# Performance work log

Measured on AMD Instinct MI355X. Metric: run time of the kernel, lower is better.

The kernel has to match this reference:

```python
import jax, jax.numpy as jnp
import numpy as np
from jax import lax

IMG = 800.0
PRE_NMS = 2000
POST_NMS = 1000
IOU_T = 0.7
BBOX_XFORM_CLIP = float(np.log(1000.0 / 16.0))


def build_anchors():
    # torchvision FPN anchor generator: one size per level, 3 aspect ratios
    strides = [4, 8, 16, 32, 64]
    sizes = [32, 64, 128, 256, 512]
    ratios = [0.5, 1.0, 2.0]
    out = []
    for s, sz in zip(strides, sizes):
        f = int(np.ceil(800 / s))  # feature map side
        base = []
        for r in ratios:
            w = sz * np.sqrt(1.0 / r)
            h = sz * np.sqrt(r)
            base.append([-w / 2, -h / 2, w / 2, h / 2])
        base = np.asarray(base)  # [3,4]
        sx = (np.arange(f) + 0.5) * s
        sy = (np.arange(f) + 0.5) * s
        yy, xx = np.meshgrid(sy, sx, indexing='ij')
        shifts = np.stack([xx, yy, xx, yy], -1).reshape(-1, 1, 4)
        out.append((shifts + base).reshape(-1, 4))
    return np.concatenate(out, 0).astype(np.float32)  # [159882,4]


def setup_inputs() -> dict:
    key = jax.random.key(0)
    k1, k2 = jax.random.split(key)
    B = 16
    anchors = jnp.asarray(build_anchors())
    A = anchors.shape[0]
    scores = jax.random.normal(k1, (B, A), dtype=jnp.float32)
    deltas = jax.random.normal(k2, (B, A, 4), dtype=jnp.float32) * 0.1
    return {"scores": scores, "deltas": deltas, "anchors": anchors}


def decode_boxes(deltas, anchors):
    wa = anchors[:, 2] - anchors[:, 0]
    ha = anchors[:, 3] - anchors[:, 1]
    cxa = anchors[:, 0] + 0.5 * wa
    cya = anchors[:, 1] + 0.5 * ha
    dx, dy = deltas[:, 0], deltas[:, 1]
    dw = jnp.minimum(deltas[:, 2], BBOX_XFORM_CLIP)
    dh = jnp.minimum(deltas[:, 3], BBOX_XFORM_CLIP)
    cx = dx * wa + cxa
    cy = dy * ha + cya
    w = jnp.exp(dw) * wa
    h = jnp.exp(dh) * ha
    boxes = jnp.stack([cx - 0.5 * w, cy - 0.5 * h, cx + 0.5 * w, cy + 0.5 * h], -1)
    return jnp.clip(boxes, 0.0, IMG)


def box_iou(a, b):
    # a: [N,4], b: [M,4]
    area_a = (a[:, 2] - a[:, 0]) * (a[:, 3] - a[:, 1])
    area_b = (b[:, 2] - b[:, 0]) * (b[:, 3] - b[:, 1])
    lt = jnp.maximum(a[:, None, :2], b[None, :, :2])
    rb = jnp.minimum(a[:, None, 2:], b[None, :, 2:])
    wh = jnp.clip(rb - lt, 0.0)
    inter = wh[..., 0] * wh[..., 1]
    return inter / (area_a[:, None] + area_b[None, :] - inter + 1e-9)


def greedy_nms_keep(boxes, iou_t):
    # boxes are sorted by descending score
    K = boxes.shape[0]
    iou = box_iou(boxes, boxes)  # [K,K]
    idx = jnp.arange(K)

    def body(i, keep):
        sup = (iou[i] > iou_t) & keep[i] & (idx > i)
        return keep & ~sup

    return lax.fori_loop(0, K, body, jnp.ones((K,), bool))


def _process_image(scores_i, deltas_i, anchors):
    # top-k pre-NMS on objectness logits (torchvision RPN order)
    top_logits, idx = lax.top_k(scores_i, PRE_NMS)
    boxes = decode_boxes(deltas_i[idx], anchors[idx])  # [PRE,4]
    keep = greedy_nms_keep(boxes, IOU_T)
    masked = jnp.where(keep, top_logits, -jnp.inf)
    kept_logits, idx2 = lax.top_k(masked, POST_NMS)
    kept_boxes = boxes[idx2]
    valid = jnp.isfinite(kept_logits)
    probs = jax.nn.sigmoid(jnp.where(valid, kept_logits, 0.0))
    out_boxes = jnp.where(valid[:, None], kept_boxes, 0.0)
    out_scores = jnp.where(valid, probs, 0.0)
    return jnp.concatenate([out_boxes, out_scores[:, None]], -1)  # [POST,5]


def reference(scores, deltas, anchors):
    return jax.vmap(_process_image, in_axes=(0, 0, None))(scores, deltas, anchors)
```

## Files before the change

kernel.cpp:

```cpp
#include <hip/hip_runtime.h>
#include <math.h>

#define PRE_NMS 2000
#define POST_NMS 1000
#define IOU_T 0.7f
#define IMGSZ 800.0f
#define CAP 6144
#define SORTN 2048
#define NBINS 1024
#define NWORDS 32
#define NSLICE 16
#define MROWS 2048
#define NTILES 528

typedef unsigned long long u64;

__device__ __forceinline__ unsigned key_of(float f) {
    unsigned u = __float_as_uint(f);
    return (u & 0x80000000u) ? ~u : (u | 0x80000000u);
}
__device__ __forceinline__ float inv_key(unsigned k) {
    unsigned u = (k & 0x80000000u) ? (k ^ 0x80000000u) : ~k;
    return __uint_as_float(u);
}

__global__ __launch_bounds__(256) void hist_kernel(
    const float* __restrict__ scores, int A, unsigned* __restrict__ ghist) {
  int b = blockIdx.x, slice = blockIdx.y;
  __shared__ unsigned h[NBINS];
  int tid = threadIdx.x;
  for (int i = tid; i < NBINS; i += 256) h[i] = 0;
  __syncthreads();
  int per = (A + NSLICE - 1) / NSLICE;
  int lo = slice * per, hi = min(lo + per, A);
  const float* sc = scores + (size_t)b * A;
  for (int i = lo + tid; i < hi; i += 256)
    atomicAdd(&h[key_of(sc[i]) >> 22], 1u);
  __syncthreads();
  for (int i = tid; i < NBINS; i += 256)
    if (h[i]) atomicAdd(&ghist[b * NBINS + i], h[i]);
}

__global__ __launch_bounds__(256) void compact_kernel(
    const float* __restrict__ scores, int A, const unsigned* __restrict__ ghist,
    u64* __restrict__ cand, int* __restrict__ cand_cnt, int* __restrict__ T1) {
  int b = blockIdx.x, slice = blockIdx.y;
  int tid = threadIdx.x;
  int lane = tid & 63, wave = tid >> 6;
  __shared__ unsigned sa[2][NBINS];
  __shared__ int sT;
  for (int i = tid; i < NBINS; i += 256) sa[0][i] = ghist[b * NBINS + i];
  __syncthreads();
  int src = 0;
  for (int d = 1; d < NBINS; d <<= 1) {
    for (int i = tid; i < NBINS; i += 256)
      sa[src ^ 1][i] = sa[src][i] + ((i + d < NBINS) ? sa[src][i + d] : 0u);
    __syncthreads();
    src ^= 1;
  }
  for (int i = tid; i < NBINS; i += 256) {
    unsigned v = sa[src][i];
    unsigned nx = (i < NBINS - 1) ? sa[src][i + 1] : 0u;
    if (v >= PRE_NMS && nx < PRE_NMS) sT = i;
  }
  __syncthreads();
  int T = sT;
  if (slice == 0 && tid == 0) T1[b] = T;
  int per = (A + NSLICE - 1) / NSLICE;
  int lo = slice * per, hi = min(lo + per, A);
  const float* sc = scores + (size_t)b * A;
  int cnt = 0;
  for (int i = lo + tid; i < hi; i += 256)
    cnt += ((int)(key_of(sc[i]) >> 22) >= T);
  int pfx = cnt;
  #pragma unroll
  for (int d = 1; d < 64; d <<= 1) {
    int t2 = __shfl_up(pfx, d, 64);
    if (lane >= d) pfx += t2;
  }
  __shared__ int s_wt[4];
  __shared__ int s_base;
  if (lane == 63) s_wt[wave] = pfx;
  __syncthreads();
  if (tid == 0) {
    int tot = s_wt[0] + s_wt[1] + s_wt[2] + s_wt[3];
    int acc = 0;
    #pragma unroll
    for (int w2 = 0; w2 < 4; ++w2) { int t3 = s_wt[w2]; s_wt[w2] = acc; acc += t3; }
    s_base = atomicAdd(&cand_cnt[b], tot);
  }
  __syncthreads();
  int my_off = s_base + s_wt[wave] + (pfx - cnt);
  u64* cb = cand + (size_t)b * CAP;
  for (int i = lo + tid; i < hi; i += 256) {
    unsigned k = key_of(sc[i]);
    if ((int)(k >> 22) >= T) {
      if (my_off < CAP) cb[my_off] = ((u64)k << 32) | (unsigned)(~i);
      my_off++;
    }
  }
}

__global__ __launch_bounds__(1024) void refine_select_kernel(
    const u64* __restrict__ cand, const int* __restrict__ cand_cnt,
    const int* __restrict__ T1,
    u64* __restrict__ gsel, int* __restrict__ sel_cnt) {
  int b = blockIdx.x, tid = threadIdx.x;
  int lane = tid & 63;
  __shared__ unsigned h2[NBINS];
  __shared__ unsigned tmp[NBINS];
  __shared__ int s_above, s_sel, s_T2;
  int n = min(cand_cnt[b], CAP);
  const u64* cb = cand + (size_t)b * CAP;
  h2[tid] = 0;
  if (tid == 0) { s_above = 0; s_sel = 0; }
  __syncthreads();
  int T1v = T1[b];
  int loc = 0;
  for (int i = tid; i < n; i += 1024) {
    unsigned k = (unsigned)(cb[i] >> 32);
    if ((int)(k >> 22) > T1v) loc++;
    else atomicAdd(&h2[(k >> 12) & 1023], 1u);
  }
  for (int d = 32; d; d >>= 1) loc += __shfl_down(loc, d, 64);
  if (lane == 0 && loc) atomicAdd(&s_above, loc);
  __syncthreads();
  unsigned v = h2[tid];
  for (int d = 1; d < NBINS; d <<= 1) {
    tmp[tid] = v;
    __syncthreads();
    if (tid + d < NBINS) v += tmp[tid + d];
    __syncthreads();
  }
  tmp[tid] = v;
  __syncthreads();
  int above = s_above;
  unsigned nextv = (tid < NBINS - 1) ? tmp[tid + 1] : 0u;
  if (above + (int)v >= PRE_NMS && above + (int)nextv < PRE_NMS) s_T2 = tid;
  __syncthreads();
  unsigned thresh20 = ((unsigned)T1v << 10) | (unsigned)s_T2;
  u64* gs = gsel + (size_t)b * SORTN;
  for (int i = tid; i < n; i += 1024) {
    u64 cv = cb[i];
    if ((unsigned)(cv >> 44) >= thresh20) {
      int pos = atomicAdd(&s_sel, 1);
      if (pos < SORTN) gs[pos] = cv;
    }
  }
  __syncthreads();
  if (tid == 0) sel_cnt[b] = min(s_sel, SORTN);
}

__global__ __launch_bounds__(256) void rank_decode_kernel(
    const u64* __restrict__ gsel, const int* __restrict__ sel_cnt,
    const float* __restrict__ deltas, const float* __restrict__ anchors, int A,
    float* __restrict__ boxes, float* __restrict__ topk_logit) {
  int b = blockIdx.x, ci = blockIdx.y;
  int tid = threadIdx.x;
  __shared__ u64 keys[SORTN];
  __shared__ int s_part[256];
  const u64* gs = gsel + (size_t)b * SORTN;
  int n = sel_cnt[b];
  for (int i = tid; i < SORTN; i += 256)
    keys[i] = (i < n) ? gs[i] : 0ULL;
  __syncthreads();
  int half = tid >> 7;
  int li = tid & 127;
  int i = ci * 128 + li;
  u64 my = keys[i];
  int rank = 0;
  const ulonglong2* k2 = (const ulonglong2*)(keys + half * (SORTN / 2));
  #pragma unroll 4
  for (int j = 0; j < SORTN / 4; ++j) {
    ulonglong2 kk = k2[j];
    rank += (kk.x > my) + (kk.y > my);
  }
  s_part[tid] = rank;
  __syncthreads();
  if (half == 0) {
    rank = s_part[tid] + s_part[tid + 128];
    if (i < n && rank < PRE_NMS) {
      int a = (int)(~(unsigned)my);
      topk_logit[b * PRE_NMS + rank] = inv_key((unsigned)(my >> 32));
      const float CLIP = 4.135166556742356f;
      float4 dl = ((const float4*)deltas)[(size_t)b * A + a];
      float4 an = ((const float4*)anchors)[a];
      float wa = __fsub_rn(an.z, an.x);
      float ha = __fsub_rn(an.w, an.y);
      float cxa = __fadd_rn(an.x, __fmul_rn(0.5f, wa));
      float cya = __fadd_rn(an.y, __fmul_rn(0.5f, ha));
      float dw = fminf(dl.z, CLIP), dh = fminf(dl.w, CLIP);
      float cx = __fadd_rn(__fmul_rn(dl.x, wa), cxa);
      float cy = __fadd_rn(__fmul_rn(dl.y, ha), cya);
      float w2 = __fmul_rn((float)exp((double)dw), wa);
      float h2f = __fmul_rn((float)exp((double)dh), ha);
      float x1 = __fsub_rn(cx, __fmul_rn(0.5f, w2));
      float y1 = __fsub_rn(cy, __fmul_rn(0.5f, h2f));
      float x2 = __fadd_rn(cx, __fmul_rn(0.5f, w2));
      float y2 = __fadd_rn(cy, __fmul_rn(0.5f, h2f));
      x1 = fminf(fmaxf(x1, 0.f), IMGSZ);
      y1 = fminf(fmaxf(y1, 0.f), IMGSZ);
      x2 = fminf(fmaxf(x2, 0.f), IMGSZ);
      y2 = fminf(fmaxf(y2, 0.f), IMGSZ);
      ((float4*)boxes)[(size_t)b * PRE_NMS + rank] = make_float4(x1, y1, x2, y2);
    }
  }
}

__global__ __launch_bounds__(64) void iou_tile(
    const float* __restrict__ boxes, u64* __restrict__ maskT,
    unsigned* __restrict__ tflag) {
  int k = blockIdx.x;
  int b = blockIdx.y;
  int wj = (int)((sqrtf(8.0f * k + 1.0f) - 1.0f) * 0.5f);
  while ((wj + 1) * (wj + 2) / 2 <= k) ++wj;
  while (wj * (wj + 1) / 2 > k) --wj;
  int ti = k - wj * (wj + 1) / 2;
  int lane = threadIdx.x;
  int i = ti * 64 + lane;
  const float4* bb = (const float4*)boxes + (size_t)b * PRE_NMS;
  __shared__ float4 sbox[64];
  int jg = wj * 64 + lane;
  sbox[lane] = bb[min(jg, PRE_NMS - 1)];
  float4 A4 = bb[min(i, PRE_NMS - 1)];
  __syncthreads();
  float area_a = __fmul_rn(__fsub_rn(A4.z, A4.x), __fsub_rn(A4.w, A4.y));
  u64 m = 0;
  #pragma unroll 8
  for (int jj = 0; jj < 64; ++jj) {
    float4 Bb = sbox[jj];
    float area_b = __fmul_rn(__fsub_rn(Bb.z, Bb.x), __fsub_rn(Bb.w, Bb.y));
    float ltx = fmaxf(A4.x, Bb.x), lty = fmaxf(A4.y, Bb.y);
    float rbx = fminf(A4.z, Bb.z), rby = fminf(A4.w, Bb.w);
    float iw = fmaxf(__fsub_rn(rbx, ltx), 0.f);
    float ih = fmaxf(__fsub_rn(rby, lty), 0.f);
    float inter = __fmul_rn(iw, ih);
    float denom = __fadd_rn(__fsub_rn(__fadd_rn(area_a, area_b), inter), 1e-9f);
    float iou = inter / denom;
    int j = wj * 64 + jj;
    if (j > i && iou > IOU_T) m |= 1ULL << jj;
  }
  maskT[((size_t)b * NWORDS + wj) * MROWS + i] = m;
  u64 anyb = __ballot(m != 0ULL);
  if (lane == 0) tflag[(size_t)b * NTILES + k] = (anyb != 0ULL) ? 1u : 0u;
}

#define WSTRIDE 65
#define BAR_LDS() asm volatile("s_waitcnt lgkmcnt(0)\n\ts_barrier" ::: "memory")
__global__ __launch_bounds__(256, 1) void nms_scan(
    const u64* __restrict__ maskT, const unsigned* __restrict__ tflag,
    const float* __restrict__ boxes,
    const float* __restrict__ logits, float* __restrict__ out) {
  int b = blockIdx.x;
  int tid = threadIdx.x;
  int wave = tid >> 6, lane = tid & 63;
  __shared__ u64 buf[3][NWORDS * WSTRIDE];
  __shared__ u64 s_keep[NWORDS];
  __shared__ u64 s_cur[2];
  __shared__ unsigned char sflag[NTILES];
  const unsigned* tf = tflag + (size_t)b * NTILES;
  for (int i2 = tid; i2 < NTILES; i2 += 256)
    sflag[i2] = (unsigned char)(tf[i2] != 0u);
  if (tid < NWORDS) s_keep[tid] = (tid == NWORDS - 1) ? 0xFFFFULL : ~0ULL;
  const u64* mb = maskT + (size_t)b * NWORDS * MROWS;
  int w = tid >> 3;
  int sub = tid & 7;
  uint4 nx0, nx1, nx2, nx3;
  {
    const uint4* src = (const uint4*)(mb + (size_t)w * MROWS + sub * 8);
    uint4 a0 = src[0], a1 = src[1], a2 = src[2], a3 = src[3];
    u64* dst = &buf[0][w * WSTRIDE + sub * 8];
    dst[0] = ((u64)a0.y << 32) | a0.x;  dst[1] = ((u64)a0.w << 32) | a0.z;
    dst[2] = ((u64)a1.y << 32) | a1.x;  dst[3] = ((u64)a1.w << 32) | a1.z;
    dst[4] = ((u64)a2.y << 32) | a2.x;  dst[5] = ((u64)a2.w << 32) | a2.z;
    dst[6] = ((u64)a3.y << 32) | a3.x;  dst[7] = ((u64)a3.w << 32) | a3.z;
  }
  bool have = (w >= 1);
  if (have) {
    const uint4* src = (const uint4*)(mb + (size_t)w * MROWS + 64 + sub * 8);
    nx0 = src[0]; nx1 = src[1]; nx2 = src[2]; nx3 = src[3];
  }
  BAR_LDS();
  for (int c = 0; c < NWORDS; ++c) {
    if (c + 1 < NWORDS && have) {
      u64* dst = &buf[(c + 1) % 3][w * WSTRIDE + sub * 8];
      dst[0] = ((u64)nx0.y << 32) | nx0.x;  dst[1] = ((u64)nx0.w << 32) | nx0.z;
      dst[2] = ((u64)nx1.y << 32) | nx1.x;  dst[3] = ((u64)nx1.w << 32) | nx1.z;
      dst[4] = ((u64)nx2.y << 32) | nx2.x;  dst[5] = ((u64)nx2.w << 32) | nx2.z;
      dst[6] = ((u64)nx3.y << 32) | nx3.x;  dst[7] = ((u64)nx3.w << 32) | nx3.z;
    }
    have = false;
    if (c + 2 < NWORDS && w >= c + 2 &&
        sflag[(w * (w + 1)) / 2 + (c + 2)]) {
      const uint4* src = (const uint4*)(mb + (size_t)w * MROWS + (c + 2) * 64 + sub * 8);
      nx0 = src[0]; nx1 = src[1]; nx2 = src[2]; nx3 = src[3];
      have = true;
    }
    if (wave == 0) {
      u64 k0 = s_keep[c];
      u64 cur;
      if (sflag[(c * (c + 3)) >> 1]) {
        u64 diag = buf[c % 3][c * WSTRIDE + lane];
        unsigned dlo = (unsigned)diag, dhi = (unsigned)(diag >> 32);
        unsigned clo = __builtin_amdgcn_readfirstlane((unsigned)k0);
        unsigned chi = __builtin_amdgcn_readfirstlane((unsigned)(k0 >> 32));
        #pragma unroll
        for (int bb = 0; bb < 32; ++bb) {
          unsigned rlo = __builtin_amdgcn_readlane(dlo, bb);
          unsigned rhi = __builtin_amdgcn_readlane(dhi, bb);
          unsigned msk = 0u - ((clo >> bb) & 1u);
          clo &= ~(rlo & msk);
          chi &= ~(rhi & msk);
        }
        #pragma unroll
        for (int bb = 0; bb < 32; ++bb) {
          unsigned rlo = __builtin_amdgcn_readlane(dlo, bb + 32);
          unsigned rhi = __builtin_amdgcn_readlane(dhi, bb + 32);
          unsigned msk = 0u - ((chi >> bb) & 1u);
          clo &= ~(rlo & msk);
          chi &= ~(rhi & msk);
        }
        cur = ((u64)chi << 32) | clo;
      } else {
        cur = k0;
      }
      if (lane == 0) { s_keep[c] = cur; s_cur[c & 1] = cur; }
      if (c + 1 < NWORDS && sflag[(((c + 1) * (c + 2)) >> 1) + c]) {
        u64 row = buf[c % 3][(c + 1) * WSTRIDE + lane];
        u64 bit = (cur >> lane) & 1ULL;
        u64 v = row & (0ULL - bit);
        v |= __shfl_xor(v, 1, 64);
        v |= __shfl_xor(v, 2, 64);
        v |= __shfl_xor(v, 4, 64);
        v |= __shfl_xor(v, 8, 64);
        v |= __shfl_xor(v, 16, 64);
        v |= __shfl_xor(v, 32, 64);
        if (lane == 0 && v) atomicAnd(&s_keep[c + 1], ~v);
      }
    } else if (c >= 1) {
      u64 kept = s_cur[(c - 1) & 1];
      int g = lane >> 3, s = lane & 7;
      const u64* bbuf = &buf[(c - 1) % 3][0];
      for (int idx = (wave - 1) + 3 * g; idx < NWORDS - 1 - c; idx += 24) {
        int w2 = c + 1 + idx;
        if (!sflag[(w2 * (w2 + 1)) / 2 + (c - 1)]) continue;
        u64 v = 0;
        #pragma unroll
        for (int k = 0; k < 8; ++k) {
          int r = s + 8 * k;
          u64 bit = (kept >> r) & 1ULL;
          v |= bbuf[w2 * WSTRIDE + r] & (0ULL - bit);
        }
        v |= __shfl_xor(v, 1, 64);
        v |= __shfl_xor(v, 2, 64);
        v |= __shfl_xor(v, 4, 64);
        if (s == 0 && v) atomicAnd(&s_keep[w2], ~v);
      }
    }
    BAR_LDS();
  }
  __shared__ int pre[NWORDS];
  __shared__ int s_tot;
  if (tid == 0) {
    int acc = 0;
    for (int ww = 0; ww < NWORDS; ++ww) {
      pre[ww] = acc;
      acc += __popcll(s_keep[ww]);
    }
    s_tot = acc;
  }
  __syncthreads();
  const float* lg_b = logits + b * PRE_NMS;
  const float4* bx_b = (const float4*)boxes + (size_t)b * PRE_NMS;
  for (int i = tid; i < PRE_NMS; i += 256) {
    u64 wv = s_keep[i >> 6];
    if ((wv >> (i & 63)) & 1) {
      int rank = pre[i >> 6] + __popcll(wv & ((1ULL << (i & 63)) - 1ULL));
      if (rank < POST_NMS) {
        float4 bx = bx_b[i];
        float lg = lg_b[i];
        float e = (float)exp(-(double)lg);
        float pp = 1.0f / (1.0f + e);
        float* o = out + ((size_t)b * POST_NMS + rank) * 5;
        o[0] = bx.x; o[1] = bx.y; o[2] = bx.z; o[3] = bx.w; o[4] = pp;
      }
    }
  }
  int tot = s_tot;
  for (int j = tid; j < POST_NMS; j += 256) {
    if (j >= tot) {
      float* o = out + ((size_t)b * POST_NMS + j) * 5;
      o[0] = 0.f; o[1] = 0.f; o[2] = 0.f; o[3] = 0.f; o[4] = 0.f;
    }
  }
}

extern "C" void kernel_launch(void* const* d_in, const int* in_sizes, int n_in,
                              void* d_out, int out_size, void* d_ws, size_t ws_size,
                              hipStream_t stream) {
  const float* scores  = (const float*)d_in[0];
  const float* deltas  = (const float*)d_in[1];
  const float* anchors = (const float*)d_in[2];
  int A = in_sizes[2] / 4;
  int B = in_sizes[0] / A;

  char* ws = (char*)d_ws;
  size_t off = 0;
  auto alloc = [&](size_t bytes) {
    void* p = ws + off;
    off += (bytes + 255) & ~(size_t)255;
    return p;
  };
  unsigned* ghist    = (unsigned*)alloc((size_t)B * NBINS * 4);
  int*      cand_cnt = (int*)alloc((size_t)B * 4);
  size_t zero_bytes = off;
  int*      T1       = (int*)alloc((size_t)B * 4);
  u64*      cand     = (u64*)alloc((size_t)B * CAP * 8);
  u64*      gsel     = (u64*)alloc((size_t)B * SORTN * 8);
  int*      sel_cnt  = (int*)alloc((size_t)B * 4);
  float*    topk_lg  = (float*)alloc((size_t)B * PRE_NMS * 4);
  float*    boxes    = (float*)alloc((size_t)B * PRE_NMS * 16);
  u64*      maskT    = (u64*)alloc((size_t)B * NWORDS * MROWS * 8);
  unsigned* tflag    = (unsigned*)alloc((size_t)B * NTILES * 4);

  hipMemsetAsync(ws, 0, zero_bytes, stream);

  hist_kernel<<<dim3(B, NSLICE), 256, 0, stream>>>(scores, A, ghist);
  compact_kernel<<<dim3(B, NSLICE), 256, 0, stream>>>(scores, A, ghist, cand, cand_cnt, T1);
  refine_select_kernel<<<B, 1024, 0, stream>>>(cand, cand_cnt, T1, gsel, sel_cnt);
  rank_decode_kernel<<<dim3(B, SORTN / 128), 256, 0, stream>>>(
      gsel, sel_cnt, deltas, anchors, A, boxes, topk_lg);
  int ntiles = NTILES;
  iou_tile<<<dim3(ntiles, B), 64, 0, stream>>>(boxes, maskT, tflag);
  nms_scan<<<B, 256, 0, stream>>>(maskT, tflag, boxes, topk_lg, (float*)d_out);
}
```

Baseline: 204.3 us.

## Stage only active NMS mask tiles and drop memset via per-slice histograms

New measurement: 205.7 us. No clear change (+0.7%).

```diff
diff --git a/kernel.cpp b/kernel.cpp
--- a/kernel.cpp
+++ b/kernel.cpp
@@ -12,6 +12,7 @@
 #define NSLICE 16
 #define MROWS 2048
 #define NTILES 528
+#define TCAP 104
 
 typedef unsigned long long u64;
 
@@ -25,11 +26,13 @@
 }
 
 __global__ __launch_bounds__(256) void hist_kernel(
-    const float* __restrict__ scores, int A, unsigned* __restrict__ ghist) {
+    const float* __restrict__ scores, int A, unsigned* __restrict__ ghist,
+    int* __restrict__ cand_cnt) {
   int b = blockIdx.x, slice = blockIdx.y;
   __shared__ unsigned h[NBINS];
   int tid = threadIdx.x;
   for (int i = tid; i < NBINS; i += 256) h[i] = 0;
+  if (slice == 0 && tid == 0) cand_cnt[b] = 0;
   __syncthreads();
   int per = (A + NSLICE - 1) / NSLICE;
   int lo = slice * per, hi = min(lo + per, A);
@@ -37,8 +40,8 @@
   for (int i = lo + tid; i < hi; i += 256)
     atomicAdd(&h[key_of(sc[i]) >> 22], 1u);
   __syncthreads();
-  for (int i = tid; i < NBINS; i += 256)
-    if (h[i]) atomicAdd(&ghist[b * NBINS + i], h[i]);
+  unsigned* gh = ghist + ((size_t)b * NSLICE + slice) * NBINS;
+  for (int i = tid; i < NBINS; i += 256) gh[i] = h[i];
 }
 
 __global__ __launch_bounds__(256) void compact_kernel(
@@ -49,7 +52,13 @@
   int lane = tid & 63, wave = tid >> 6;
   __shared__ unsigned sa[2][NBINS];
   __shared__ int sT;
-  for (int i = tid; i < NBINS; i += 256) sa[0][i] = ghist[b * NBINS + i];
+  for (int i = tid; i < NBINS; i += 256) {
+    unsigned s = 0;
+    const unsigned* gh = ghist + (size_t)b * NSLICE * NBINS + i;
+    #pragma unroll
+    for (int s16 = 0; s16 < NSLICE; ++s16) s += gh[s16 * NBINS];
+    sa[0][i] = s;
+  }
   __syncthreads();
   int src = 0;
   for (int d = 1; d < NBINS; d <<= 1) {
@@ -236,74 +245,74 @@
     float ih = fmaxf(__fsub_rn(rby, lty), 0.f);
     float inter = __fmul_rn(iw, ih);
     float denom = __fadd_rn(__fsub_rn(__fadd_rn(area_a, area_b), inter), 1e-9f);
-    float iou = inter / denom;
     int j = wj * 64 + jj;
-    if (j > i && iou > IOU_T) m |= 1ULL << jj;
-  }
-  maskT[((size_t)b * NWORDS + wj) * MROWS + i] = m;
+    if (j > i && inter > __fmul_rn(IOU_T, denom)) m |= 1ULL << jj;
+  }
   u64 anyb = __ballot(m != 0ULL);
+  if (anyb) maskT[((size_t)b * NWORDS + wj) * MROWS + i] = m;
   if (lane == 0) tflag[(size_t)b * NTILES + k] = (anyb != 0ULL) ? 1u : 0u;
 }
 
-#define WSTRIDE 65
-#define BAR_LDS() asm volatile("s_waitcnt lgkmcnt(0)\n\ts_barrier" ::: "memory")
 __global__ __launch_bounds__(256, 1) void nms_scan(
     const u64* __restrict__ maskT, const unsigned* __restrict__ tflag,
     const float* __restrict__ boxes,
     const float* __restrict__ logits, float* __restrict__ out) {
   int b = blockIdx.x;
   int tid = threadIdx.x;
-  int wave = tid >> 6, lane = tid & 63;
-  __shared__ u64 buf[3][NWORDS * WSTRIDE];
+  int lane = tid & 63, wave = tid >> 6;
+  __shared__ u64 tiles[TCAP][64];
+  __shared__ unsigned wflags[NWORDS];
+  __shared__ int wbase[NWORDS];
+  __shared__ unsigned short slot2cw[TCAP];
+  __shared__ int s_nact;
   __shared__ u64 s_keep[NWORDS];
-  __shared__ u64 s_cur[2];
-  __shared__ unsigned char sflag[NTILES];
+  __shared__ int pre[NWORDS];
+  __shared__ int s_tot;
   const unsigned* tf = tflag + (size_t)b * NTILES;
-  for (int i2 = tid; i2 < NTILES; i2 += 256)
-    sflag[i2] = (unsigned char)(tf[i2] != 0u);
-  if (tid < NWORDS) s_keep[tid] = (tid == NWORDS - 1) ? 0xFFFFULL : ~0ULL;
   const u64* mb = maskT + (size_t)b * NWORDS * MROWS;
-  int w = tid >> 3;
-  int sub = tid & 7;
-  uint4 nx0, nx1, nx2, nx3;
-  {
-    const uint4* src = (const uint4*)(mb + (size_t)w * MROWS + sub * 8);
-    uint4 a0 = src[0], a1 = src[1], a2 = src[2], a3 = src[3];
-    u64* dst = &buf[0][w * WSTRIDE + sub * 8];
-    dst[0] = ((u64)a0.y << 32) | a0.x;  dst[1] = ((u64)a0.w << 32) | a0.z;
-    dst[2] = ((u64)a1.y << 32) | a1.x;  dst[3] = ((u64)a1.w << 32) | a1.z;
-    dst[4] = ((u64)a2.y << 32) | a2.x;  dst[5] = ((u64)a2.w << 32) | a2.z;
-    dst[6] = ((u64)a3.y << 32) | a3.x;  dst[7] = ((u64)a3.w << 32) | a3.z;
-  }
-  bool have = (w >= 1);
-  if (have) {
-    const uint4* src = (const uint4*)(mb + (size_t)w * MROWS + 64 + sub * 8);
-    nx0 = src[0]; nx1 = src[1]; nx2 = src[2]; nx3 = src[3];
-  }
-  BAR_LDS();
-  for (int c = 0; c < NWORDS; ++c) {
-    if (c + 1 < NWORDS && have) {
-      u64* dst = &buf[(c + 1) % 3][w * WSTRIDE + sub * 8];
-      dst[0] = ((u64)nx0.y << 32) | nx0.x;  dst[1] = ((u64)nx0.w << 32) | nx0.z;
-      dst[2] = ((u64)nx1.y << 32) | nx1.x;  dst[3] = ((u64)nx1.w << 32) | nx1.z;
-      dst[4] = ((u64)nx2.y << 32) | nx2.x;  dst[5] = ((u64)nx2.w << 32) | nx2.z;
-      dst[6] = ((u64)nx3.y << 32) | nx3.x;  dst[7] = ((u64)nx3.w << 32) | nx3.z;
-    }
-    have = false;
-    if (c + 2 < NWORDS && w >= c + 2 &&
-        sflag[(w * (w + 1)) / 2 + (c + 2)]) {
-      const uint4* src = (const uint4*)(mb + (size_t)w * MROWS + (c + 2) * 64 + sub * 8);
-      nx0 = src[0]; nx1 = src[1]; nx2 = src[2]; nx3 = src[3];
-      have = true;
-    }
-    if (wave == 0) {
-      u64 k0 = s_keep[c];
-      u64 cur;
-      if (sflag[(c * (c + 3)) >> 1]) {
-        u64 diag = buf[c % 3][c * WSTRIDE + lane];
-        unsigned dlo = (unsigned)diag, dhi = (unsigned)(diag >> 32);
-        unsigned clo = __builtin_amdgcn_readfirstlane((unsigned)k0);
-        unsigned chi = __builtin_amdgcn_readfirstlane((unsigned)(k0 >> 32));
+  if (tid < NWORDS) {
+    int c = tid;
+    unsigned wf = 0;
+    for (int w2 = c; w2 < NWORDS; ++w2)
+      if (tf[w2 * (w2 + 1) / 2 + c]) wf |= 1u << w2;
+    wflags[c] = wf;
+  }
+  __syncthreads();
+  if (tid == 0) {
+    int s = 0;
+    for (int c = 0; c < NWORDS; ++c) {
+      wbase[c] = s;
+      unsigned wf = wflags[c];
+      while (wf) {
+        int w2 = __ffs(wf) - 1; wf &= wf - 1;
+        if (s < TCAP) slot2cw[s] = (unsigned short)((w2 << 8) | c);
+        s++;
+      }
+    }
+    s_nact = s;
+  }
+  __syncthreads();
+  int nstage = min(s_nact, TCAP);
+  for (int g = tid; g < nstage * 64; g += 256) {
+    int slot = g >> 6, r = g & 63;
+    unsigned cw = slot2cw[slot];
+    int c = cw & 0xFF, w2 = cw >> 8;
+    tiles[slot][r] = mb[(size_t)w2 * MROWS + c * 64 + r];
+  }
+  __syncthreads();
+  if (wave == 0) {
+    u64 keep = (lane < NWORDS) ? ((lane == NWORDS - 1) ? 0xFFFFULL : ~0ULL) : 0ULL;
+    for (int c = 0; c < NWORDS; ++c) {
+      unsigned wf = wflags[c];
+      int base = wbase[c];
+      u64 cur = __shfl(keep, c, 64);
+      if ((wf >> c) & 1u) {
+        int slot = base;
+        u64 d = (slot < TCAP) ? tiles[slot][lane]
+                              : mb[(size_t)c * MROWS + c * 64 + lane];
+        unsigned dlo = (unsigned)d, dhi = (unsigned)(d >> 32);
+        unsigned clo = __builtin_amdgcn_readfirstlane((unsigned)cur);
+        unsigned chi = __builtin_amdgcn_readfirstlane((unsigned)(cur >> 32));
         #pragma unroll
         for (int bb = 0; bb < 32; ++bb) {
           unsigned rlo = __builtin_amdgcn_readlane(dlo, bb);
@@ -321,12 +330,14 @@
           chi &= ~(rhi & msk);
         }
         cur = ((u64)chi << 32) | clo;
-      } else {
-        cur = k0;
+        keep = (lane == c) ? cur : keep;
       }
-      if (lane == 0) { s_keep[c] = cur; s_cur[c & 1] = cur; }
-      if (c + 1 < NWORDS && sflag[(((c + 1) * (c + 2)) >> 1) + c]) {
-        u64 row = buf[c % 3][(c + 1) * WSTRIDE + lane];
+      unsigned rem = wf & ~((2u << c) - 1u);
+      while (rem) {
+        int w2 = __ffs(rem) - 1; rem &= rem - 1;
+        int slot = base + __popc(wf & ((1u << w2) - 1u));
+        u64 row = (slot < TCAP) ? tiles[slot][lane]
+                                : mb[(size_t)w2 * MROWS + c * 64 + lane];
         u64 bit = (cur >> lane) & 1ULL;
         u64 v = row & (0ULL - bit);
         v |= __shfl_xor(v, 1, 64);
@@ -335,32 +346,12 @@
         v |= __shfl_xor(v, 8, 64);
         v |= __shfl_xor(v, 16, 64);
         v |= __shfl_xor(v, 32, 64);
-        if (lane == 0 && v) atomicAnd(&s_keep[c + 1], ~v);
+        keep = (lane == w2) ? (keep & ~v) : keep;
       }
-    } else if (c >= 1) {
-      u64 kept = s_cur[(c - 1) & 1];
-      int g = lane >> 3, s = lane & 7;
-      const u64* bbuf = &buf[(c - 1) % 3][0];
-      for (int idx = (wave - 1) + 3 * g; idx < NWORDS - 1 - c; idx += 24) {
-        int w2 = c + 1 + idx;
-        if (!sflag[(w2 * (w2 + 1)) / 2 + (c - 1)]) continue;
-        u64 v = 0;
-        #pragma unroll
-        for (int k = 0; k < 8; ++k) {
-          int r = s + 8 * k;
-          u64 bit = (kept >> r) & 1ULL;
-          v |= bbuf[w2 * WSTRIDE + r] & (0ULL - bit);
-        }
-        v |= __shfl_xor(v, 1, 64);
-        v |= __shfl_xor(v, 2, 64);
-        v |= __shfl_xor(v, 4, 64);
-        if (s == 0 && v) atomicAnd(&s_keep[w2], ~v);
-      }
-    }
-    BAR_LDS();
-  }
-  __shared__ int pre[NWORDS];
-  __shared__ int s_tot;
+    }
+    if (lane < NWORDS) s_keep[lane] = keep;
+  }
+  __syncthreads();
   if (tid == 0) {
     int acc = 0;
     for (int ww = 0; ww < NWORDS; ++ww) {
@@ -411,9 +402,8 @@
     off += (bytes + 255) & ~(size_t)255;
     return p;
   };
-  unsigned* ghist    = (unsigned*)alloc((size_t)B * NBINS * 4);
+  unsigned* ghist    = (unsigned*)alloc((size_t)B * NSLICE * NBINS * 4);
   int*      cand_cnt = (int*)alloc((size_t)B * 4);
-  size_t zero_bytes = off;
   int*      T1       = (int*)alloc((size_t)B * 4);
   u64*      cand     = (u64*)alloc((size_t)B * CAP * 8);
   u64*      gsel     = (u64*)alloc((size_t)B * SORTN * 8);
@@ -423,14 +413,11 @@
   u64*      maskT    = (u64*)alloc((size_t)B * NWORDS * MROWS * 8);
   unsigned* tflag    = (unsigned*)alloc((size_t)B * NTILES * 4);
 
-  hipMemsetAsync(ws, 0, zero_bytes, stream);
-
-  hist_kernel<<<dim3(B, NSLICE), 256, 0, stream>>>(scores, A, ghist);
+  hist_kernel<<<dim3(B, NSLICE), 256, 0, stream>>>(scores, A, ghist, cand_cnt);
   compact_kernel<<<dim3(B, NSLICE), 256, 0, stream>>>(scores, A, ghist, cand, cand_cnt, T1);
   refine_select_kernel<<<B, 1024, 0, stream>>>(cand, cand_cnt, T1, gsel, sel_cnt);
   rank_decode_kernel<<<dim3(B, SORTN / 128), 256, 0, stream>>>(
       gsel, sel_cnt, deltas, anchors, A, boxes, topk_lg);
-  int ntiles = NTILES;
-  iou_tile<<<dim3(ntiles, B), 64, 0, stream>>>(boxes, maskT, tflag);
+  iou_tile<<<dim3(NTILES, B), 64, 0, stream>>>(boxes, maskT, tflag);
   nms_scan<<<B, 256, 0, stream>>>(maskT, tflag, boxes, topk_lg, (float*)d_out);
 }
```
